# Kernel optimization log

Measured on AMD Instinct MI355X. Metric: run time of the kernel, lower is better.

## Reference

```python
import jax, jax.numpy as jnp
import numpy as np

B, S, D, O, R, E = 2, 4096, 4096, 4096, 256, 8
SCALE = 2.0

def setup_inputs() -> dict:
    key = jax.random.key(0)
    k_x, k_t, k_w, k_a, k_b = jax.random.split(key, 5)
    x = jax.random.normal(k_x, (B, S, D), dtype=jnp.float32)
    token_type = jax.random.randint(k_t, (S,), 0, E, dtype=jnp.int64)
    # weight_base: [out_features, in_features] as required by F.linear
    weight_base = jax.random.normal(k_w, (O, D), dtype=jnp.float32) * 0.02
    # LoRA stacks: lora_A [E, D, R], lora_B [E, R, O]. (Original inits B to zeros;
    # we use small random values so the LoRA path is numerically non-trivial.)
    lora_A = jax.random.normal(k_a, (E, D, R), dtype=jnp.float32) * 0.02
    lora_B = jax.random.normal(k_b, (E, R, O), dtype=jnp.float32) * 0.02
    return {"x": x, "weight_base": weight_base, "lora_A": lora_A,
            "lora_B": lora_B, "token_type": token_type}

def reference(x, weight_base, lora_A, lora_B, token_type):
    # base GEMM: F.linear(x, W) = x @ W.T  -> [B, S, O]
    base = jnp.einsum('bsd,od->bso', x, weight_base)
    # per-expert low-rank projection: h[e,b,s,:] = x[b,s,:] @ lora_A[e]
    h = jnp.einsum('bsd,edr->ebsr', x, lora_A)              # [E, B, S, R]
    # dispatch: zero out tokens not routed to expert e (token_type partitions S)
    onehot = jax.nn.one_hot(token_type, E, dtype=x.dtype)   # [S, E]
    h = h * onehot.T[:, None, :, None]                      # mask over (e, s)
    # combine: sum over experts of masked h @ lora_B[e]
    lora = jnp.einsum('ebsr,ero->bso', h, lora_B)           # [B, S, O]
    # every token has token_type in [0, E), so scatter covers all positions:
    # result = base + scale * expert_lora everywhere
    return base + SCALE * lora
```

## Files before the change

### kernel.cpp

```cpp
#include <hip/hip_runtime.h>

#define S_TOK 4096
#define D_DIM 4096
#define O_DIM 4096
#define R_DIM 256
#define E_EXP 8
#define NTOK  8192
#define KSPLIT 4

typedef __bf16 bf16x8 __attribute__((ext_vector_type(8)));
typedef float  f32x4  __attribute__((ext_vector_type(4)));

__device__ __forceinline__ unsigned short f2bf(float f) {
  unsigned int u = __float_as_uint(f);
  u += 0x7FFFu + ((u >> 16) & 1u);
  return (unsigned short)(u >> 16);
}
__device__ __forceinline__ float bf2f(unsigned short h) {
  return __uint_as_float(((unsigned int)h) << 16);
}

__device__ __forceinline__ void gload_lds16(const unsigned short* g, unsigned short* l) {
  __builtin_amdgcn_global_load_lds((const __attribute__((address_space(1))) void*)g,
                                   (__attribute__((address_space(3))) void*)l, 16, 0, 0);
}

#define PIPE_FENCE(N)                                                        \
  do {                                                                       \
    asm volatile("s_waitcnt vmcnt(" #N ")\n\ts_barrier" ::: "memory");       \
    __builtin_amdgcn_sched_barrier(0);                                       \
  } while (0)
#define BARX                                                                 \
  do {                                                                       \
    asm volatile("s_barrier" ::: "memory");                                  \
    __builtin_amdgcn_sched_barrier(0);                                       \
  } while (0)

__global__ void prologue(const float* __restrict__ x, const float* __restrict__ wb,
                         const float* __restrict__ la, const float* __restrict__ lb,
                         unsigned short* __restrict__ X16, unsigned short* __restrict__ W16,
                         unsigned short* __restrict__ A16t, unsigned short* __restrict__ B16t,
                         const int* __restrict__ tt, int* __restrict__ token_perm,
                         int* __restrict__ tile_e, int* __restrict__ tile_j0,
                         int* __restrict__ tile_jend, int* __restrict__ ntiles_out,
                         int* __restrict__ seg_n, int* __restrict__ seg_e,
                         int* __restrict__ seg_lo, int* __restrict__ seg_hi,
                         unsigned short* __restrict__ zp) {
  __shared__ int sm[10256];
  const int b = blockIdx.x, t = threadIdx.x;
  if (b >= 40960) {
    int* ltt   = sm;
    int* lc    = sm + 4096;
    int* ssl   = sm + 6144;
    int* basee = sm + 10240;
    int* cnte  = sm + 10248;
    if (t < 64) ((long long*)zp)[t] = 0;
    for (int s = t; s < S_TOK; s += 256) ltt[s] = tt[s];
    __syncthreads();
    int c[8] = {0,0,0,0,0,0,0,0};
    #pragma unroll
    for (int i = 0; i < 16; i++) { int e = ltt[t * 16 + i]; c[e]++; }
    #pragma unroll
    for (int e = 0; e < 8; e++) lc[t * 8 + e] = c[e];
    __syncthreads();
    if (t < 8) {
      int run = 0;
      for (int qq = 0; qq < 256; qq++) { int tmp = lc[qq * 8 + t]; lc[qq * 8 + t] = run; run += tmp; }
      cnte[t] = run;
    }
    __syncthreads();
    if (t == 0) { int tot = 0; for (int e = 0; e < 8; e++) { basee[e] = tot; tot += cnte[e]; } }
    __syncthreads();
    int off[8];
    #pragma unroll
    for (int e = 0; e < 8; e++) off[e] = basee[e] + lc[t * 8 + e];
    #pragma unroll
    for (int i = 0; i < 16; i++) { int s = t * 16 + i; int e = ltt[s]; ssl[off[e]++] = s; }
    __syncthreads();
    for (int j = t; j < NTOK; j += 256) {
      token_perm[j] = ((j & 1) << 12) + ssl[j >> 1];
    }
    if (t == 0) {
      int nt = 0;
      for (int e = 0; e < 8; e++) {
        int js = 2 * basee[e], je = js + 2 * cnte[e];
        for (int j0 = js; j0 < je; j0 += 128) {
          tile_e[nt] = e; tile_j0[nt] = j0;
          tile_jend[nt] = (je < j0 + 128) ? je : (j0 + 128);
          nt++;
        }
      }
      *ntiles_out = nt;
      for (int p = 0; p < 32; p++) {
        int plo = p * 256, phi = plo + 256, ns = 0;
        for (int e = 0; e < 8; e++) {
          int es = 2 * basee[e], ee = es + 2 * cnte[e];
          int lo = es > plo ? es : plo;
          int hi = ee < phi ? ee : phi;
          if (lo < hi) { seg_e[p * 8 + ns] = e; seg_lo[p * 8 + ns] = lo - plo;
                         seg_hi[p * 8 + ns] = hi - plo; ns++; }
        }
        seg_n[p] = ns;
      }
    }
    return;
  }
  if (b < 24576) {
    const float* in  = (b < 16384) ? x : wb;
    unsigned short* out = (b < 16384) ? X16 : W16;
    size_t g = (size_t)((b < 16384) ? b : (b - 16384)) * 256 + t;
    const float4* i4 = (const float4*)in;
    float4 a = i4[g * 2], c = i4[g * 2 + 1];
    union { unsigned short h[8]; int4 v; } u;
    u.h[0] = f2bf(a.x); u.h[1] = f2bf(a.y); u.h[2] = f2bf(a.z); u.h[3] = f2bf(a.w);
    u.h[4] = f2bf(c.x); u.h[5] = f2bf(c.y); u.h[6] = f2bf(c.z); u.h[7] = f2bf(c.w);
    ((int4*)out)[g] = u.v;
    return;
  }
  unsigned short (*tile)[33] = (unsigned short (*)[33])sm;
  const float* in; unsigned short* out; int P, Q, pt, qt, e;
  if (b < 32768) {
    int b2 = b - 24576; e = b2 >> 10; int rem = b2 & 1023;
    in = la; out = A16t; P = D_DIM; Q = R_DIM;
    pt = (rem >> 3) * 32; qt = (rem & 7) * 32;
  } else {
    int b3 = b - 32768; e = b3 >> 10; int rem = b3 & 1023;
    in = lb; out = B16t; P = R_DIM; Q = D_DIM;
    pt = (rem & 7) * 32; qt = (rem >> 3) * 32;
  }
  const float* ie = in + (size_t)e * P * Q;
  unsigned short* oe = out + (size_t)e * P * Q;
  int tx = t & 31, ty = t >> 5;
  #pragma unroll
  for (int i = 0; i < 32; i += 8) {
    int p = pt + ty + i, q = qt + tx;
    tile[ty + i][tx] = f2bf(ie[(size_t)p * Q + q]);
  }
  __syncthreads();
  #pragma unroll
  for (int i = 0; i < 32; i += 8) {
    int q = qt + ty + i, p = pt + tx;
    oe[(size_t)q * P + p] = tile[tx][ty + i];
  }
}

__global__ __launch_bounds__(512, 2) void gemm256_s(
    const unsigned short* __restrict__ A, const unsigned short* __restrict__ B,
    const unsigned short* __restrict__ H, const unsigned short* __restrict__ Bl,
    float* __restrict__ C, const int* __restrict__ perm,
    const int* __restrict__ seg_n, const int* __restrict__ seg_e,
    const int* __restrict__ seg_lo, const int* __restrict__ seg_hi,
    const unsigned short* __restrict__ zp) {
  __shared__ __align__(16) unsigned short ldsA[2][2][8192];
  __shared__ __align__(16) unsigned short ldsB[2][2][8192];
  int b = blockIdx.x;
  int xc = b & 7, q = b >> 3;
  const int bm = (xc >> 1) * 8 + (q >> 3);
  const int bn = (xc & 1) * 8 + (q & 7);
  const int tid = threadIdx.x, l = tid & 63, w = tid >> 6;
  const int wm = w >> 2, wn = w & 3;

  const int i0 = tid, r0 = i0 >> 2;
  const int c0 = ((i0 & 3) * 16) ^ (((r0 >> 1) & 3) << 4);
  const int i1 = 512 + tid, r1 = i1 >> 2;
  const int c1 = ((i1 & 3) * 16) ^ (((r1 >> 1) & 3) << 4);
  const int sr0 = perm[bm * 256 + r0];
  const int sr1 = perm[bm * 256 + r1];
  const unsigned short* srcA0 = A + (size_t)sr0 * 4096 + (c0 >> 1);
  const unsigned short* srcA1 = A + (size_t)sr1 * 4096 + (c1 >> 1);
  const unsigned short* srcB0 = B + (size_t)(bn * 256 + r0) * 4096 + (c0 >> 1);
  const unsigned short* srcB1 = B + (size_t)(bn * 256 + r1) * 4096 + (c1 >> 1);

  const int lane15 = l & 15, kb16 = (l >> 4) * 16;
  int offA[8], offB[4];
  #pragma unroll
  for (int m = 0; m < 8; m++) {
    int r = wm * 128 + m * 16 + lane15;
    offA[m] = r * 64 + (kb16 ^ (((r >> 1) & 3) << 4));
  }
  #pragma unroll
  for (int n = 0; n < 4; n++) {
    int r = wn * 64 + n * 16 + lane15;
    offB[n] = r * 64 + (kb16 ^ (((r >> 1) & 3) << 4));
  }

  f32x4 acc[8][4];
  #pragma unroll
  for (int m = 0; m < 8; m++)
    #pragma unroll
    for (int n = 0; n < 4; n++) acc[m][n] = (f32x4){0.f, 0.f, 0.f, 0.f};

  bf16x8 Ab0[4], Ab1[4], Bb0[4], Bb1[4];

#define STAGE_A(tt, kh) do { int _o = (tt) * 64 + (kh) * 32;                  \
    gload_lds16(srcA0 + _o, &ldsA[(tt) & 1][kh][tid * 8]);                    \
    gload_lds16(srcA1 + _o, &ldsA[(tt) & 1][kh][tid * 8 + 4096]); } while (0)
#define STAGE_B(tt, kh) do { int _o = (tt) * 64 + (kh) * 32;                  \
    gload_lds16(srcB0 + _o, &ldsB[(tt) & 1][kh][tid * 8]);                    \
    gload_lds16(srcB1 + _o, &ldsB[(tt) & 1][kh][tid * 8 + 4096]); } while (0)
#define RD_A(RING, QQ, KS, BUF) do {                                          \
    const char* _s = (const char*)&ldsA[RING][KS][0];                         \
    BUF[0] = *(const bf16x8*)(_s + offA[(QQ) * 4 + 0]);                       \
    BUF[1] = *(const bf16x8*)(_s + offA[(QQ) * 4 + 1]);                       \
    BUF[2] = *(const bf16x8*)(_s + offA[(QQ) * 4 + 2]);                       \
    BUF[3] = *(const bf16x8*)(_s + offA[(QQ) * 4 + 3]); } while (0)
#define RD_B(RING, KS, BUF) do {                                              \
    const char* _s = (const char*)&ldsB[RING][KS][0];                         \
    BUF[0] = *(const bf16x8*)(_s + offB[0]);                                  \
    BUF[1] = *(const bf16x8*)(_s + offB[1]);                                  \
    BUF[2] = *(const bf16x8*)(_s + offB[2]);                                  \
    BUF[3] = *(const bf16x8*)(_s + offB[3]); } while (0)
#define PRIO_MFMA(Q, AB, BB) do {                                             \
    __builtin_amdgcn_s_setprio(1);                                            \
    _Pragma("unroll")                                                         \
    for (int mm = 0; mm < 4; mm++)                                            \
      _Pragma("unroll")                                                       \
      for (int nn = 0; nn < 4; nn++)                                          \
        acc[(Q) * 4 + mm][nn] = __builtin_amdgcn_mfma_f32_16x16x32_bf16(      \
            AB[mm], BB[nn], acc[(Q) * 4 + mm][nn], 0, 0, 0);                  \
    __builtin_amdgcn_s_setprio(0); } while (0)

  STAGE_A(0, 0); STAGE_B(0, 0); STAGE_A(0, 1); STAGE_B(0, 1);
  STAGE_A(1, 0); STAGE_B(1, 0);
  PIPE_FENCE(4);
  RD_B(0, 0, Bb0); RD_A(0, 0, 0, Ab0);

  #pragma unroll 1
  for (int t = 0; t < 62; ++t) {
    const int r = t & 1, nr = r ^ 1;
    RD_A(r, 1, 0, Ab1); STAGE_A(t + 1, 1);
    PRIO_MFMA(0, Ab0, Bb0);
    RD_B(r, 1, Bb1); RD_A(r, 0, 1, Ab0); STAGE_B(t + 1, 1);
    PRIO_MFMA(1, Ab1, Bb0);
    PIPE_FENCE(4);
    RD_A(r, 1, 1, Ab1); STAGE_A(t + 2, 0);
    PRIO_MFMA(0, Ab0, Bb1);
    RD_B(nr, 0, Bb0); RD_A(nr, 0, 0, Ab0); STAGE_B(t + 2, 0);
    PRIO_MFMA(1, Ab1, Bb1);
    PIPE_FENCE(4);
  }
  RD_A(0, 1, 0, Ab1); STAGE_A(63, 1); PRIO_MFMA(0, Ab0, Bb0);
  RD_B(0, 1, Bb1); RD_A(0, 0, 1, Ab0); STAGE_B(63, 1); PRIO_MFMA(1, Ab1, Bb0);
  PIPE_FENCE(4);
  RD_A(0, 1, 1, Ab1); PRIO_MFMA(0, Ab0, Bb1);
  RD_B(1, 0, Bb0); RD_A(1, 0, 0, Ab0); PRIO_MFMA(1, Ab1, Bb1);
  PIPE_FENCE(0);
  RD_A(1, 1, 0, Ab1); PRIO_MFMA(0, Ab0, Bb0);
  RD_B(1, 1, Bb1); RD_A(1, 0, 1, Ab0); PRIO_MFMA(1, Ab1, Bb0);
  RD_A(1, 1, 1, Ab1); PRIO_MFMA(0, Ab0, Bb1);
  PRIO_MFMA(1, Ab1, Bb1);

  const int pn = seg_n[bm];
  #pragma unroll 1
  for (int s = 0; s < pn; ++s) {
    const int eE = seg_e[bm * 8 + s], lo = seg_lo[bm * 8 + s], hi = seg_hi[bm * 8 + s];
    const unsigned short* h0 = (r0 >= lo && r0 < hi)
        ? H + (size_t)(bm * 256 + r0) * 256 + (c0 >> 1) : zp + (c0 >> 1);
    const unsigned short* h1 = (r1 >= lo && r1 < hi)
        ? H + (size_t)(bm * 256 + r1) * 256 + (c1 >> 1) : zp + (c1 >> 1);
    const unsigned short* be0 = Bl + (size_t)eE * (O_DIM * R_DIM)
        + (size_t)(bn * 256 + r0) * 256 + (c0 >> 1);
    const unsigned short* be1 = Bl + (size_t)eE * (O_DIM * R_DIM)
        + (size_t)(bn * 256 + r1) * 256 + (c1 >> 1);
    #pragma unroll 1
    for (int kt = 0; kt < 4; ++kt) {
      const int rg = kt & 1;
      const int o0 = kt * 64, o1 = kt * 64 + 32;
      gload_lds16(h0 + o0,  &ldsA[rg][0][tid * 8]);
      gload_lds16(h1 + o0,  &ldsA[rg][0][tid * 8 + 4096]);
      gload_lds16(h0 + o1,  &ldsA[rg][1][tid * 8]);
      gload_lds16(h1 + o1,  &ldsA[rg][1][tid * 8 + 4096]);
      gload_lds16(be0 + o0, &ldsB[rg][0][tid * 8]);
      gload_lds16(be1 + o0, &ldsB[rg][0][tid * 8 + 4096]);
      gload_lds16(be0 + o1, &ldsB[rg][1][tid * 8]);
      gload_lds16(be1 + o1, &ldsB[rg][1][tid * 8 + 4096]);
      PIPE_FENCE(0);
      RD_B(rg, 0, Bb0); RD_A(rg, 0, 0, Ab0); PRIO_MFMA(0, Ab0, Bb0);
      RD_A(rg, 1, 0, Ab1);                   PRIO_MFMA(1, Ab1, Bb0);
      RD_B(rg, 1, Bb1); RD_A(rg, 0, 1, Ab0); PRIO_MFMA(0, Ab0, Bb1);
      RD_A(rg, 1, 1, Ab1);                   PRIO_MFMA(1, Ab1, Bb1);
      BARX;
    }
  }

#undef STAGE_A
#undef STAGE_B
#undef RD_A
#undef RD_B
#undef PRIO_MFMA

  const int rowbase = bm * 256 + wm * 128;
  const int colbase = bn * 256 + wn * 64;
  #pragma unroll
  for (int m = 0; m < 8; m++)
    #pragma unroll
    for (int v = 0; v < 4; v++) {
      int rrow = rowbase + m * 16 + (l >> 4) * 4 + v;
      int orow = perm[rrow];
      size_t base = (size_t)orow * O_DIM + colbase + lane15;
      C[base]      = acc[m][0][v];
      C[base + 16] = acc[m][1][v];
      C[base + 32] = acc[m][2][v];
      C[base + 48] = acc[m][3][v];
    }
}

__global__ __launch_bounds__(256, 2) void gemm_nt1(
    const unsigned short* __restrict__ Aop, const unsigned short* __restrict__ Bop,
    unsigned short* __restrict__ outU,
    const int* __restrict__ perm, const int* __restrict__ tile_e,
    const int* __restrict__ tile_j0, const int* __restrict__ tile_jend,
    const int* __restrict__ ntiles) {
  const int K = D_DIM;
  int bm = blockIdx.x, bn = blockIdx.y;
  if (bm >= *ntiles) return;
  int e = tile_e[bm], j0 = tile_j0[bm], jend = tile_jend[bm];
  const int kc = blockIdx.z;
  const int t = threadIdx.x, l = t & 63, w = t >> 6;
  const int wm = w >> 1, wn = w & 1;
  __shared__ __align__(16) unsigned short ldsA[4][4096];
  __shared__ __align__(16) unsigned short ldsB[4][4096];

  const unsigned short *sA0, *sA1, *sB0, *sB1;
  {
    int i0 = t, r0 = i0 >> 2;
    int c0 = ((i0 & 3) * 16) ^ (((r0 >> 1) & 3) << 4);
    int i1 = 256 + t, r1 = i1 >> 2;
    int c1 = ((i1 & 3) * 16) ^ (((r1 >> 1) & 3) << 4);
    int ja = j0 + r0; if (ja > jend - 1) ja = jend - 1;
    int jb = j0 + r1; if (jb > jend - 1) jb = jend - 1;
    int g0 = perm[ja], g1 = perm[jb];
    sA0 = Aop + (size_t)g0 * K + kc * 1024 + (c0 >> 1);
    sA1 = Aop + (size_t)g1 * K + kc * 1024 + (c1 >> 1);
    const unsigned short* bp = Bop + (size_t)e * R_DIM * D_DIM;
    sB0 = bp + (size_t)(bn * 128 + r0) * K + kc * 1024 + (c0 >> 1);
    sB1 = bp + (size_t)(bn * 128 + r1) * K + kc * 1024 + (c1 >> 1);
  }
  const int d0 = t * 8;

  const int lane15 = l & 15, kb16 = (l >> 4) * 16;
  int offA[4], offB[4];
  #pragma unroll
  for (int m = 0; m < 4; m++) {
    int r = wm * 64 + m * 16 + lane15;
    offA[m] = r * 64 + (kb16 ^ (((r >> 1) & 3) << 4));
  }
  #pragma unroll
  for (int n = 0; n < 4; n++) {
    int r = wn * 64 + n * 16 + lane15;
    offB[n] = r * 64 + (kb16 ^ (((r >> 1) & 3) << 4));
  }

  f32x4 acc[4][4];
  #pragma unroll
  for (int m = 0; m < 4; m++)
    #pragma unroll
    for (int n = 0; n < 4; n++) acc[m][n] = (f32x4){0.f, 0.f, 0.f, 0.f};

  auto stage = [&](int tt) {
    const int ring = tt & 3;
    const int go = tt * 32;
    gload_lds16(sA0 + go, &ldsA[ring][d0]);
    gload_lds16(sA1 + go, &ldsA[ring][d0 + 2048]);
    gload_lds16(sB0 + go, &ldsB[ring][d0]);
    gload_lds16(sB1 + go, &ldsB[ring][d0 + 2048]);
  };

  auto body = [&](int ring) {
    const char* bA = (const char*)&ldsA[ring][0];
    const char* bB = (const char*)&ldsB[ring][0];
    bf16x8 a[4], bb[4];
    #pragma unroll
    for (int m = 0; m < 4; m++) a[m] = *(const bf16x8*)(bA + offA[m]);
    #pragma unroll
    for (int n = 0; n < 4; n++) bb[n] = *(const bf16x8*)(bB + offB[n]);
    __builtin_amdgcn_s_setprio(1);
    #pragma unroll
    for (int m = 0; m < 4; m++)
      #pragma unroll
      for (int n = 0; n < 4; n++)
        acc[m][n] = __builtin_amdgcn_mfma_f32_16x16x32_bf16(a[m], bb[n], acc[m][n], 0, 0, 0);
    __builtin_amdgcn_s_setprio(0);
  };

  const int nk = 32;
  stage(0); stage(1); stage(2);
  PIPE_FENCE(8);
  #pragma unroll 1
  for (int kt = 0; kt < nk - 3; ++kt) {
    stage(kt + 3);
    body(kt & 3);
    PIPE_FENCE(8);
  }
  body((nk - 3) & 3);
  PIPE_FENCE(4);
  body((nk - 2) & 3);
  PIPE_FENCE(0);
  body((nk - 1) & 3);

  const int rowbase = j0 + wm * 64;
  const int colbase = bn * 128 + wn * 64;
  #pragma unroll
  for (int m = 0; m < 4; m++) {
    #pragma unroll
    for (int n = 0; n < 4; n++) {
      #pragma unroll
      for (int v = 0; v < 4; v++) {
        int r = rowbase + m * 16 + (l >> 4) * 4 + v;
        int cc = colbase + n * 16 + lane15;
        if (r < jend)
          outU[(size_t)kc * (NTOK * R_DIM) + (size_t)r * R_DIM + cc] = f2bf(acc[m][n][v]);
      }
    }
  }
}

__global__ void reduce_h(const unsigned short* __restrict__ hp, unsigned short* __restrict__ h16) {
  size_t g = (size_t)blockIdx.x * 256 + threadIdx.x;
  float s[8] = {0,0,0,0,0,0,0,0};
  #pragma unroll
  for (int c = 0; c < KSPLIT; c++) {
    int4 v = ((const int4*)hp)[g + (size_t)c * (NTOK * R_DIM / 8)];
    const unsigned short* us = (const unsigned short*)&v;
    #pragma unroll
    for (int i = 0; i < 8; i++) s[i] += bf2f(us[i]);
  }
  union { unsigned short h[8]; int4 v; } u;
  #pragma unroll
  for (int i = 0; i < 8; i++) u.h[i] = f2bf(2.0f * s[i]);
  ((int4*)h16)[g] = u.v;
}

#define X16_OFF   ((size_t)0)
#define W16_OFF   ((size_t)67108864)
#define A16T_OFF  ((size_t)100663296)
#define B16T_OFF  ((size_t)117440512)
#define H16S_OFF  ((size_t)134217728)
#define PERM_OFF  ((size_t)138412032)
#define TILEE_OFF ((size_t)138477568)
#define TILEJ0_OFF ((size_t)138478080)
#define TILEJE_OFF ((size_t)138478592)
#define NT_OFF    ((size_t)138479104)
#define HP16_OFF  ((size_t)138479616)
#define SEGN_OFF  ((size_t)155256832)
#define SEGE_OFF  ((size_t)155257344)
#define SEGLO_OFF ((size_t)155258368)
#define SEGHI_OFF ((size_t)155259392)
#define ZERO_OFF  ((size_t)155260416)

extern "C" void kernel_launch(void* const* d_in, const int* in_sizes, int n_in,
                              void* d_out, int out_size, void* d_ws, size_t ws_size,
                              hipStream_t stream) {
  const float* x  = (const float*)d_in[0];
  const float* wb = (const float*)d_in[1];
  const float* la = (const float*)d_in[2];
  const float* lb = (const float*)d_in[3];
  const int* tok  = (const int*)d_in[4];
  float* out = (float*)d_out;

  char* ws = (char*)d_ws;
  unsigned short* X16  = (unsigned short*)(ws + X16_OFF);
  unsigned short* W16  = (unsigned short*)(ws + W16_OFF);
  unsigned short* A16t = (unsigned short*)(ws + A16T_OFF);
  unsigned short* B16t = (unsigned short*)(ws + B16T_OFF);
  unsigned short* H16s = (unsigned short*)(ws + H16S_OFF);
  unsigned short* HP16 = (unsigned short*)(ws + HP16_OFF);
  unsigned short* ZP   = (unsigned short*)(ws + ZERO_OFF);
  int* perm  = (int*)(ws + PERM_OFF);
  int* tl_e  = (int*)(ws + TILEE_OFF);
  int* tl_j0 = (int*)(ws + TILEJ0_OFF);
  int* tl_je = (int*)(ws + TILEJE_OFF);
  int* nt    = (int*)(ws + NT_OFF);
  int* sgn   = (int*)(ws + SEGN_OFF);
  int* sge   = (int*)(ws + SEGE_OFF);
  int* sglo  = (int*)(ws + SEGLO_OFF);
  int* sghi  = (int*)(ws + SEGHI_OFF);

  prologue<<<40961, 256, 0, stream>>>(x, wb, la, lb, X16, W16, A16t, B16t,
                                      tok, perm, tl_e, tl_j0, tl_je, nt,
                                      sgn, sge, sglo, sghi, ZP);

  gemm_nt1<<<dim3(71, 2, KSPLIT), 256, 0, stream>>>(X16, A16t, HP16,
                                                    perm, tl_e, tl_j0, tl_je, nt);
  reduce_h<<<1024, 256, 0, stream>>>(HP16, H16s);

  gemm256_s<<<512, 512, 0, stream>>>(X16, W16, H16s, B16t, out, perm,
                                     sgn, sge, sglo, sghi, ZP);
}
```

Before: 405.3 us.

## Drop reduce_h kernel by consuming split-K partials directly in LoRA-B GEMM

```diff
diff --git a/kernel.cpp b/kernel.cpp
--- a/kernel.cpp
+++ b/kernel.cpp
@@ -6,7 +6,7 @@
 #define R_DIM 256
 #define E_EXP 8
 #define NTOK  8192
-#define KSPLIT 4
+#define KSPLIT 2
 
 typedef __bf16 bf16x8 __attribute__((ext_vector_type(8)));
 typedef float  f32x4  __attribute__((ext_vector_type(4)));
@@ -146,7 +146,7 @@
 
 __global__ __launch_bounds__(512, 2) void gemm256_s(
     const unsigned short* __restrict__ A, const unsigned short* __restrict__ B,
-    const unsigned short* __restrict__ H, const unsigned short* __restrict__ Bl,
+    const unsigned short* __restrict__ HP, const unsigned short* __restrict__ Bl,
     float* __restrict__ C, const int* __restrict__ perm,
     const int* __restrict__ seg_n, const int* __restrict__ seg_e,
     const int* __restrict__ seg_lo, const int* __restrict__ seg_hi,
@@ -254,32 +254,37 @@
   #pragma unroll 1
   for (int s = 0; s < pn; ++s) {
     const int eE = seg_e[bm * 8 + s], lo = seg_lo[bm * 8 + s], hi = seg_hi[bm * 8 + s];
-    const unsigned short* h0 = (r0 >= lo && r0 < hi)
-        ? H + (size_t)(bm * 256 + r0) * 256 + (c0 >> 1) : zp + (c0 >> 1);
-    const unsigned short* h1 = (r1 >= lo && r1 < hi)
-        ? H + (size_t)(bm * 256 + r1) * 256 + (c1 >> 1) : zp + (c1 >> 1);
     const unsigned short* be0 = Bl + (size_t)eE * (O_DIM * R_DIM)
         + (size_t)(bn * 256 + r0) * 256 + (c0 >> 1);
     const unsigned short* be1 = Bl + (size_t)eE * (O_DIM * R_DIM)
         + (size_t)(bn * 256 + r1) * 256 + (c1 >> 1);
     #pragma unroll 1
-    for (int kt = 0; kt < 4; ++kt) {
-      const int rg = kt & 1;
-      const int o0 = kt * 64, o1 = kt * 64 + 32;
-      gload_lds16(h0 + o0,  &ldsA[rg][0][tid * 8]);
-      gload_lds16(h1 + o0,  &ldsA[rg][0][tid * 8 + 4096]);
-      gload_lds16(h0 + o1,  &ldsA[rg][1][tid * 8]);
-      gload_lds16(h1 + o1,  &ldsA[rg][1][tid * 8 + 4096]);
-      gload_lds16(be0 + o0, &ldsB[rg][0][tid * 8]);
-      gload_lds16(be1 + o0, &ldsB[rg][0][tid * 8 + 4096]);
-      gload_lds16(be0 + o1, &ldsB[rg][1][tid * 8]);
-      gload_lds16(be1 + o1, &ldsB[rg][1][tid * 8 + 4096]);
-      PIPE_FENCE(0);
-      RD_B(rg, 0, Bb0); RD_A(rg, 0, 0, Ab0); PRIO_MFMA(0, Ab0, Bb0);
-      RD_A(rg, 1, 0, Ab1);                   PRIO_MFMA(1, Ab1, Bb0);
-      RD_B(rg, 1, Bb1); RD_A(rg, 0, 1, Ab0); PRIO_MFMA(0, Ab0, Bb1);
-      RD_A(rg, 1, 1, Ab1);                   PRIO_MFMA(1, Ab1, Bb1);
-      BARX;
+    for (int kc = 0; kc < KSPLIT; ++kc) {
+      const unsigned short* h0 = (r0 >= lo && r0 < hi)
+          ? HP + (size_t)kc * (NTOK * R_DIM) + (size_t)(bm * 256 + r0) * 256 + (c0 >> 1)
+          : zp + (c0 >> 1);
+      const unsigned short* h1 = (r1 >= lo && r1 < hi)
+          ? HP + (size_t)kc * (NTOK * R_DIM) + (size_t)(bm * 256 + r1) * 256 + (c1 >> 1)
+          : zp + (c1 >> 1);
+      #pragma unroll 1
+      for (int kt = 0; kt < 4; ++kt) {
+        const int rg = kt & 1;
+        const int o0 = kt * 64, o1 = kt * 64 + 32;
+        gload_lds16(h0 + o0,  &ldsA[rg][0][tid * 8]);
+        gload_lds16(h1 + o0,  &ldsA[rg][0][tid * 8 + 4096]);
+        gload_lds16(h0 + o1,  &ldsA[rg][1][tid * 8]);
+        gload_lds16(h1 + o1,  &ldsA[rg][1][tid * 8 + 4096]);
+        gload_lds16(be0 + o0, &ldsB[rg][0][tid * 8]);
+        gload_lds16(be1 + o0, &ldsB[rg][0][tid * 8 + 4096]);
+        gload_lds16(be0 + o1, &ldsB[rg][1][tid * 8]);
+        gload_lds16(be1 + o1, &ldsB[rg][1][tid * 8 + 4096]);
+        PIPE_FENCE(0);
+        RD_B(rg, 0, Bb0); RD_A(rg, 0, 0, Ab0); PRIO_MFMA(0, Ab0, Bb0);
+        RD_A(rg, 1, 0, Ab1);                   PRIO_MFMA(1, Ab1, Bb0);
+        RD_B(rg, 1, Bb1); RD_A(rg, 0, 1, Ab0); PRIO_MFMA(0, Ab0, Bb1);
+        RD_A(rg, 1, 1, Ab1);                   PRIO_MFMA(1, Ab1, Bb1);
+        BARX;
+      }
     }
   }
 
@@ -330,11 +335,11 @@
     int ja = j0 + r0; if (ja > jend - 1) ja = jend - 1;
     int jb = j0 + r1; if (jb > jend - 1) jb = jend - 1;
     int g0 = perm[ja], g1 = perm[jb];
-    sA0 = Aop + (size_t)g0 * K + kc * 1024 + (c0 >> 1);
-    sA1 = Aop + (size_t)g1 * K + kc * 1024 + (c1 >> 1);
+    sA0 = Aop + (size_t)g0 * K + kc * 2048 + (c0 >> 1);
+    sA1 = Aop + (size_t)g1 * K + kc * 2048 + (c1 >> 1);
     const unsigned short* bp = Bop + (size_t)e * R_DIM * D_DIM;
-    sB0 = bp + (size_t)(bn * 128 + r0) * K + kc * 1024 + (c0 >> 1);
-    sB1 = bp + (size_t)(bn * 128 + r1) * K + kc * 1024 + (c1 >> 1);
+    sB0 = bp + (size_t)(bn * 128 + r0) * K + kc * 2048 + (c0 >> 1);
+    sB1 = bp + (size_t)(bn * 128 + r1) * K + kc * 2048 + (c1 >> 1);
   }
   const int d0 = t * 8;
 
@@ -383,7 +388,7 @@
     __builtin_amdgcn_s_setprio(0);
   };
 
-  const int nk = 32;
+  const int nk = 64;
   stage(0); stage(1); stage(2);
   PIPE_FENCE(8);
   #pragma unroll 1
@@ -409,33 +414,16 @@
         int r = rowbase + m * 16 + (l >> 4) * 4 + v;
         int cc = colbase + n * 16 + lane15;
         if (r < jend)
-          outU[(size_t)kc * (NTOK * R_DIM) + (size_t)r * R_DIM + cc] = f2bf(acc[m][n][v]);
+          outU[(size_t)kc * (NTOK * R_DIM) + (size_t)r * R_DIM + cc] = f2bf(2.0f * acc[m][n][v]);
       }
     }
   }
-}
-
-__global__ void reduce_h(const unsigned short* __restrict__ hp, unsigned short* __restrict__ h16) {
-  size_t g = (size_t)blockIdx.x * 256 + threadIdx.x;
-  float s[8] = {0,0,0,0,0,0,0,0};
-  #pragma unroll
-  for (int c = 0; c < KSPLIT; c++) {
-    int4 v = ((const int4*)hp)[g + (size_t)c * (NTOK * R_DIM / 8)];
-    const unsigned short* us = (const unsigned short*)&v;
-    #pragma unroll
-    for (int i = 0; i < 8; i++) s[i] += bf2f(us[i]);
-  }
-  union { unsigned short h[8]; int4 v; } u;
-  #pragma unroll
-  for (int i = 0; i < 8; i++) u.h[i] = f2bf(2.0f * s[i]);
-  ((int4*)h16)[g] = u.v;
 }
 
 #define X16_OFF   ((size_t)0)
 #define W16_OFF   ((size_t)67108864)
 #define A16T_OFF  ((size_t)100663296)
 #define B16T_OFF  ((size_t)117440512)
-#define H16S_OFF  ((size_t)134217728)
 #define PERM_OFF  ((size_t)138412032)
 #define TILEE_OFF ((size_t)138477568)
 #define TILEJ0_OFF ((size_t)138478080)
@@ -463,7 +451,6 @@
   unsigned short* W16  = (unsigned short*)(ws + W16_OFF);
   unsigned short* A16t = (unsigned short*)(ws + A16T_OFF);
   unsigned short* B16t = (unsigned short*)(ws + B16T_OFF);
-  unsigned short* H16s = (unsigned short*)(ws + H16S_OFF);
   unsigned short* HP16 = (unsigned short*)(ws + HP16_OFF);
   unsigned short* ZP   = (unsigned short*)(ws + ZERO_OFF);
   int* perm  = (int*)(ws + PERM_OFF);
@@ -482,8 +469,7 @@
 
   gemm_nt1<<<dim3(71, 2, KSPLIT), 256, 0, stream>>>(X16, A16t, HP16,
                                                     perm, tl_e, tl_j0, tl_je, nt);
-  reduce_h<<<1024, 256, 0, stream>>>(HP16, H16s);
-
-  gemm256_s<<<512, 512, 0, stream>>>(X16, W16, H16s, B16t, out, perm,
+
+  gemm256_s<<<512, 512, 0, stream>>>(X16, W16, HP16, B16t, out, perm,
                                      sgn, sge, sglo, sghi, ZP);
 }
```

Result: slower. 422.3 us (+4.2%).
